# Kernel tuning notes

Measured on AMD Instinct MI355X. Metric: run time of the kernel, lower is better.

Reference implementation:

```python
import jax, jax.numpy as jnp
import numpy as np

B, T, F, U = 256, 2048, 64, 64
KEEP = 0.5  # recurrent_dropout=0.5 -> keep prob 0.5


def setup_inputs() -> dict:
    key = jax.random.key(0)
    ks = jax.random.split(key, 7)
    inputs = jax.random.normal(ks[0], (B, T, F), dtype=jnp.float32)
    kernel = jax.random.normal(ks[1], (F, 3 * U), dtype=jnp.float32) * 0.1
    recurrent_kernel = jax.random.normal(ks[2], (U, 3 * U), dtype=jnp.float32) * 0.1
    bias = jax.random.normal(ks[3], (2, 3 * U), dtype=jnp.float32) * 0.1
    dense_w = jax.random.normal(ks[4], (U, 1), dtype=jnp.float32) * 0.1
    dense_b = jnp.zeros((1,), dtype=jnp.float32)
    # Keras recurrent dropout: one fixed mask per gate (z, r, h), constant over time,
    # applied to h_prev before the recurrent matmul; inverted-dropout scaling.
    bern = jax.random.bernoulli(ks[5], KEEP, (3, B, U)).astype(jnp.float32)
    rec_mask = bern / KEEP
    return {
        "inputs": inputs,
        "kernel": kernel,
        "recurrent_kernel": recurrent_kernel,
        "bias": bias,
        "dense_w": dense_w,
        "dense_b": dense_b,
        "rec_mask": rec_mask,
    }


def _gru_dense(inputs, kernel, recurrent_kernel, bias, dense_w, dense_b, rec_mask):
    # Precompute input projections for all timesteps: [B, T, 3U]
    x_proj = jnp.einsum("btf,fg->btg", inputs, kernel) + bias[0]
    Uz, Ur, Uh = jnp.split(recurrent_kernel, 3, axis=1)  # each [U, U]
    bz, br, bh = jnp.split(bias[1], 3)                   # each [U]
    mz, mr, mh = rec_mask[0], rec_mask[1], rec_mask[2]   # each [B, U]

    def step(h, xt):
        xz, xr, xh = jnp.split(xt, 3, axis=-1)  # each [B, U]
        z = jax.nn.sigmoid(xz + (h * mz) @ Uz + bz)
        r = jax.nn.sigmoid(xr + (h * mr) @ Ur + br)
        hh = jnp.tanh(xh + r * ((h * mh) @ Uh + bh))  # reset_after=True
        h_new = z * h + (1.0 - z) * hh
        return h_new, None

    h0 = jnp.zeros((B, U), dtype=inputs.dtype)
    h_last, _ = jax.lax.scan(step, h0, jnp.swapaxes(x_proj, 0, 1))  # scan over T
    return h_last @ dense_w + dense_b  # [B, 1]


def reference(inputs, kernel, recurrent_kernel, bias, dense_w, dense_b, rec_mask):
    return _gru_dense(inputs, kernel, recurrent_kernel, bias, dense_w, dense_b, rec_mask)
```

## Files before the change

kernel.cpp:

```cpp
#include <hip/hip_runtime.h>

#define BB 256
#define TT 2048
#define FF 64
#define UU 64
#define C3 192
#define CH 32
#define NCH (TT / CH)

__device__ __forceinline__ float fast_sigmoid(float x) {
    return __builtin_amdgcn_rcpf(1.0f + __expf(-x));
}
__device__ __forceinline__ float fast_tanh(float x) {
    return 1.0f - 2.0f * __builtin_amdgcn_rcpf(__expf(2.0f * x) + 1.0f);
}
__device__ __forceinline__ float shflx(float v, int m) { return __shfl_xor(v, m, 64); }

#define REP16(M) M(0) M(1) M(2) M(3) M(4) M(5) M(6) M(7) \
                 M(8) M(9) M(10) M(11) M(12) M(13) M(14) M(15)

__global__ void __launch_bounds__(256, 1)
gru_v7(const float* __restrict__ in, const float* __restrict__ kmat,
       const float* __restrict__ rk, const float* __restrict__ bias,
       const float* __restrict__ mask, const float* __restrict__ dw,
       const float* __restrict__ db, float* __restrict__ out) {
    __shared__ __align__(16) float hb[2][64];
    __shared__ __align__(16) float ab[2][CH][FF];

    const int b    = blockIdx.x;
    const int lane = threadIdx.x & 63;
    const int wv   = threadIdx.x >> 6;
    const int sub  = lane >> 4;
    const int u    = lane & 15;
    const int j    = (wv << 4) + u;
    const int i0   = sub << 4;

    const float* mzp = mask;
    const float* mrp = mask + (size_t)BB * UU;
    const float* mhp = mask + (size_t)2 * BB * UU;
#define DECLW(K) float uz##K, ur##K, uh##K, kz##K, kr##K, kh##K;
    REP16(DECLW)
#define INITW(K) { const int i_ = i0 + (K); \
    uz##K = rk[i_ * C3 + j]       * mzp[(size_t)b * UU + i_]; \
    ur##K = rk[i_ * C3 + 64 + j]  * mrp[(size_t)b * UU + i_]; \
    uh##K = rk[i_ * C3 + 128 + j] * mhp[(size_t)b * UU + i_]; \
    kz##K = kmat[i_ * C3 + j]; \
    kr##K = kmat[i_ * C3 + 64 + j]; \
    kh##K = kmat[i_ * C3 + 128 + j]; }
    REP16(INITW)

    const float bzj  = bias[j]       + bias[C3 + j];
    const float brj  = bias[64 + j]  + bias[C3 + 64 + j];
    const float bh0j = bias[128 + j];
    const float bh1j = bias[C3 + 128 + j];

    const float* __restrict__ inb = in + (size_t)b * TT * FF;

    {
        const float* src = inb + (size_t)(wv * 8) * FF + lane;
        const float t0 = src[0 * FF], t1 = src[1 * FF], t2 = src[2 * FF],
                    t3 = src[3 * FF], t4 = src[4 * FF], t5 = src[5 * FF],
                    t6 = src[6 * FF], t7 = src[7 * FF];
        float* dst = &ab[0][wv * 8][lane];
        dst[0 * FF] = t0; dst[1 * FF] = t1; dst[2 * FF] = t2; dst[3 * FF] = t3;
        dst[4 * FF] = t4; dst[5 * FF] = t5; dst[6 * FF] = t6; dst[7 * FF] = t7;
    }
    if (wv == 0) hb[0][lane] = 0.0f;
    __syncthreads();

    float4 aA = *(const float4*)&ab[0][0][i0];
    float4 aB = *(const float4*)&ab[0][0][i0 + 4];
    float4 aC = *(const float4*)&ab[0][0][i0 + 8];
    float4 aD = *(const float4*)&ab[0][0][i0 + 12];

    float hown = 0.0f;

#pragma unroll 1
    for (int e = 0; e < TT; ++e) {
        const int  c  = e >> 5;
        const bool st = ((e & 31) == 0) && (c + 1 < NCH);

        float g0, g1, g2, g3, g4, g5, g6, g7;
        if (st) {
            const float* src = inb + ((size_t)(c + 1) * CH + wv * 8) * FF + lane;
            g0 = src[0 * FF]; g1 = src[1 * FF]; g2 = src[2 * FF]; g3 = src[3 * FF];
            g4 = src[4 * FF]; g5 = src[5 * FF]; g6 = src[6 * FF]; g7 = src[7 * FF];
        }

        const float4 hA = *(const float4*)&hb[e & 1][i0];
        const float4 hB = *(const float4*)&hb[e & 1][i0 + 4];
        const float4 hC = *(const float4*)&hb[e & 1][i0 + 8];
        const float4 hD = *(const float4*)&hb[e & 1][i0 + 12];

        float az = 0.f, ar = 0.f, axh = 0.f;
#define FMA_A(K, AV) { az = fmaf(AV, kz##K, az); ar = fmaf(AV, kr##K, ar); \
                       axh = fmaf(AV, kh##K, axh); }
        FMA_A(0,  aA.x) FMA_A(1,  aA.y) FMA_A(2,  aA.z) FMA_A(3,  aA.w)
        FMA_A(4,  aB.x) FMA_A(5,  aB.y) FMA_A(6,  aB.z) FMA_A(7,  aB.w)
        FMA_A(8,  aC.x) FMA_A(9,  aC.y) FMA_A(10, aC.z) FMA_A(11, aC.w)
        FMA_A(12, aD.x) FMA_A(13, aD.y) FMA_A(14, aD.z) FMA_A(15, aD.w)

        float hz = 0.f, hr = 0.f, hah = 0.f;
#define FMA_H(K, HV) { hz = fmaf(HV, uz##K, hz); hr = fmaf(HV, ur##K, hr); \
                       hah = fmaf(HV, uh##K, hah); }
        FMA_H(0,  hA.x) FMA_H(1,  hA.y) FMA_H(2,  hA.z) FMA_H(3,  hA.w)
        FMA_H(4,  hB.x) FMA_H(5,  hB.y) FMA_H(6,  hB.z) FMA_H(7,  hB.w)
        FMA_H(8,  hC.x) FMA_H(9,  hC.y) FMA_H(10, hC.z) FMA_H(11, hC.w)
        FMA_H(12, hD.x) FMA_H(13, hD.y) FMA_H(14, hD.z) FMA_H(15, hD.w)

        float sz = az + hz, sr = ar + hr, sxh = axh, sah = hah;
        { const float t0 = shflx(sz, 16), t1 = shflx(sr, 16),
                      t2 = shflx(sxh, 16), t3 = shflx(sah, 16);
          sz += t0; sr += t1; sxh += t2; sah += t3; }
        { const float t0 = shflx(sz, 32), t1 = shflx(sr, 32),
                      t2 = shflx(sxh, 32), t3 = shflx(sah, 32);
          sz += t0; sr += t1; sxh += t2; sah += t3; }

        const float z  = fast_sigmoid(sz + bzj);
        const float r  = fast_sigmoid(sr + brj);
        const float hh = fast_tanh(fmaf(r, sah + bh1j, sxh + bh0j));
        hown = fmaf(z, hown - hh, hh);

        if (sub == 0) hb[(e + 1) & 1][j] = hown;

        const int rn = (e + 1 < TT) ? (e + 1) : (TT - 1);
        const float* ap = &ab[(rn >> 5) & 1][rn & (CH - 1)][i0];
        aA = *(const float4*)(ap);
        aB = *(const float4*)(ap + 4);
        aC = *(const float4*)(ap + 8);
        aD = *(const float4*)(ap + 12);

        if (st) {
            float* dst = &ab[(c + 1) & 1][wv * 8][lane];
            dst[0 * FF] = g0; dst[1 * FF] = g1; dst[2 * FF] = g2; dst[3 * FF] = g3;
            dst[4 * FF] = g4; dst[5 * FF] = g5; dst[6 * FF] = g6; dst[7 * FF] = g7;
        }

        __syncthreads();
    }

    if (wv == 0) {
        float p = hb[0][lane] * dw[lane];
#pragma unroll
        for (int o = 32; o > 0; o >>= 1) p += __shfl_down(p, o, 64);
        if (lane == 0) out[b] = p + db[0];
    }
}

extern "C" void kernel_launch(void* const* d_in, const int* in_sizes, int n_in,
                              void* d_out, int out_size, void* d_ws, size_t ws_size,
                              hipStream_t stream) {
    (void)in_sizes; (void)n_in; (void)d_ws; (void)ws_size; (void)out_size;
    const float* inputs = (const float*)d_in[0];
    const float* kmat   = (const float*)d_in[1];
    const float* rk     = (const float*)d_in[2];
    const float* bias   = (const float*)d_in[3];
    const float* dw     = (const float*)d_in[4];
    const float* db     = (const float*)d_in[5];
    const float* mask   = (const float*)d_in[6];
    float* out = (float*)d_out;

    gru_v7<<<BB, 256, 0, stream>>>(inputs, kmat, rk, bias, mask, dw, db, out);
}
```

Baseline: 1.062 ms.

## Split input projection into a separate parallel kernel ahead of the recurrent scan

Computes the input projection x@K+bias for all timesteps in a separate wide-grid kernel that writes to workspace, in time chunks sized to fit the workspace. The scan kernel then only does the recurrent matmul per step and reads precomputed gate inputs from a shared-memory ring. This removes 48 FMAs per step from the serial critical path and frees registers. The cost is extra global traffic for the B*T*192 projection buffer and extra launches. If the workspace is too small it falls back to the fused kernel.

New measurement: 1.159 ms. +9.1%, slower.

```diff
diff --git a/kernel.cpp b/kernel.cpp
--- a/kernel.cpp
+++ b/kernel.cpp
@@ -5,9 +5,11 @@
 #define FF 64
 #define UU 64
 #define C3 192
-#define CH 32
-#define NCH (TT / CH)
-
+#define CH 16
+
+__device__ __forceinline__ float readlane_f(float v, int lane) {
+    return __int_as_float(__builtin_amdgcn_readlane(__float_as_int(v), lane));
+}
 __device__ __forceinline__ float fast_sigmoid(float x) {
     return __builtin_amdgcn_rcpf(1.0f + __expf(-x));
 }
@@ -18,14 +20,154 @@
 
 #define REP16(M) M(0) M(1) M(2) M(3) M(4) M(5) M(6) M(7) \
                  M(8) M(9) M(10) M(11) M(12) M(13) M(14) M(15)
+#define XREP8(M, I) M(I,0) M(I,1) M(I,2) M(I,3) M(I,4) M(I,5) M(I,6) M(I,7)
+#define XREP64(M) XREP8(M,0) XREP8(M,1) XREP8(M,2) XREP8(M,3) \
+                  XREP8(M,4) XREP8(M,5) XREP8(M,6) XREP8(M,7)
+
+__global__ __launch_bounds__(256)
+void xproj(const float* __restrict__ in, const float* __restrict__ kmat,
+           const float* __restrict__ bias, float* __restrict__ xp,
+           int t0, int tc) {
+    const int lane = threadIdx.x & 63;
+    const int wave = (int)((blockIdx.x * blockDim.x + threadIdx.x) >> 6);
+    const int nwaves = (int)((gridDim.x * blockDim.x) >> 6);
+
+#define DECLK(I,J) float kz_##I##J, kr_##I##J, kh_##I##J;
+    XREP64(DECLK)
+#define INITK(I,J) { const int f_ = (I)*8+(J); \
+    kz_##I##J = kmat[f_ * C3 + lane]; \
+    kr_##I##J = kmat[f_ * C3 + 64 + lane]; \
+    kh_##I##J = kmat[f_ * C3 + 128 + lane]; }
+    XREP64(INITK)
+
+    const float bz  = bias[lane]       + bias[C3 + lane];
+    const float br  = bias[64 + lane]  + bias[C3 + 64 + lane];
+    const float bh0 = bias[128 + lane];
+
+    const int rows = BB * tc;
+    for (int r = wave; r < rows; r += nwaves) {
+        const int bq = r / tc;
+        const int t  = t0 + (r - bq * tc);
+        const float a = in[((size_t)bq * TT + t) * FF + lane];
+        float az = bz, ar = br, ah = bh0;
+#define STEPK(I,J) { const float s_ = readlane_f(a, (I)*8+(J)); \
+        az = fmaf(s_, kz_##I##J, az); ar = fmaf(s_, kr_##I##J, ar); \
+        ah = fmaf(s_, kh_##I##J, ah); }
+        XREP64(STEPK)
+        float* o = xp + (size_t)r * C3;
+        o[lane] = az; o[64 + lane] = ar; o[128 + lane] = ah;
+    }
+}
 
 __global__ void __launch_bounds__(256, 1)
-gru_v7(const float* __restrict__ in, const float* __restrict__ kmat,
-       const float* __restrict__ rk, const float* __restrict__ bias,
-       const float* __restrict__ mask, const float* __restrict__ dw,
-       const float* __restrict__ db, float* __restrict__ out) {
+gru_scan(const float* __restrict__ xp, const float* __restrict__ rk,
+         const float* __restrict__ bias, const float* __restrict__ mask,
+         const float* __restrict__ dw, const float* __restrict__ db,
+         float* __restrict__ hws, float* __restrict__ out,
+         int tc, int first, int last) {
     __shared__ __align__(16) float hb[2][64];
-    __shared__ __align__(16) float ab[2][CH][FF];
+    __shared__ __align__(16) float ring[2][CH][C3];
+
+    const int b    = blockIdx.x;
+    const int tid  = threadIdx.x;
+    const int lane = tid & 63;
+    const int wv   = tid >> 6;
+    const int sub  = lane >> 4;
+    const int u    = lane & 15;
+    const int j    = (wv << 4) + u;
+    const int i0   = sub << 4;
+
+    const float* mzp = mask;
+    const float* mrp = mask + (size_t)BB * UU;
+    const float* mhp = mask + (size_t)2 * BB * UU;
+#define DECLUW(K) float uz##K, ur##K, uh##K;
+    REP16(DECLUW)
+#define INITUW(K) { const int i_ = i0 + (K); \
+    uz##K = rk[i_ * C3 + j]       * mzp[(size_t)b * UU + i_]; \
+    ur##K = rk[i_ * C3 + 64 + j]  * mrp[(size_t)b * UU + i_]; \
+    uh##K = rk[i_ * C3 + 128 + j] * mhp[(size_t)b * UU + i_]; }
+    REP16(INITUW)
+
+    const float bh1j = bias[C3 + 128 + j];
+
+    const float* __restrict__ xpb = xp + (size_t)b * tc * C3;
+
+    {
+        const float4* src = (const float4*)xpb;
+        const float4 v0 = src[tid], v1 = src[tid + 256], v2 = src[tid + 512];
+        float4* dst = (float4*)&ring[0][0][0];
+        dst[tid] = v0; dst[tid + 256] = v1; dst[tid + 512] = v2;
+    }
+    float hown = first ? 0.0f : hws[(size_t)b * UU + j];
+    if (wv == 0) hb[0][lane] = first ? 0.0f : hws[(size_t)b * UU + lane];
+    __syncthreads();
+
+#pragma unroll 1
+    for (int e = 0; e < tc; ++e) {
+        const int  c  = e >> 4;
+        const bool st = ((e & 15) == 0) && ((c + 1) * CH < tc);
+
+        float4 g0, g1, g2;
+        if (st) {
+            const float4* src = (const float4*)(xpb + (size_t)(c + 1) * CH * C3);
+            g0 = src[tid]; g1 = src[tid + 256]; g2 = src[tid + 512];
+        }
+
+        const float4 hA = *(const float4*)&hb[e & 1][i0];
+        const float4 hB = *(const float4*)&hb[e & 1][i0 + 4];
+        const float4 hC = *(const float4*)&hb[e & 1][i0 + 8];
+        const float4 hD = *(const float4*)&hb[e & 1][i0 + 12];
+
+        const float* xrow = &ring[c & 1][e & 15][0];
+        const float xz = xrow[j], xr = xrow[64 + j], xh = xrow[128 + j];
+
+        float hz = 0.f, hr = 0.f, hah = 0.f;
+#define FMA_H(K, HV) { hz = fmaf(HV, uz##K, hz); hr = fmaf(HV, ur##K, hr); \
+                       hah = fmaf(HV, uh##K, hah); }
+        FMA_H(0,  hA.x) FMA_H(1,  hA.y) FMA_H(2,  hA.z) FMA_H(3,  hA.w)
+        FMA_H(4,  hB.x) FMA_H(5,  hB.y) FMA_H(6,  hB.z) FMA_H(7,  hB.w)
+        FMA_H(8,  hC.x) FMA_H(9,  hC.y) FMA_H(10, hC.z) FMA_H(11, hC.w)
+        FMA_H(12, hD.x) FMA_H(13, hD.y) FMA_H(14, hD.z) FMA_H(15, hD.w)
+
+        float sz = hz, sr = hr, sah = hah;
+        { const float t0 = shflx(sz, 16), t1 = shflx(sr, 16), t2 = shflx(sah, 16);
+          sz += t0; sr += t1; sah += t2; }
+        { const float t0 = shflx(sz, 32), t1 = shflx(sr, 32), t2 = shflx(sah, 32);
+          sz += t0; sr += t1; sah += t2; }
+
+        const float z  = fast_sigmoid(sz + xz);
+        const float r  = fast_sigmoid(sr + xr);
+        const float hh = fast_tanh(fmaf(r, sah + bh1j, xh));
+        hown = fmaf(z, hown - hh, hh);
+
+        if (sub == 0) hb[(e + 1) & 1][j] = hown;
+
+        if (st) {
+            float4* dst = (float4*)&ring[(c + 1) & 1][0][0];
+            dst[tid] = g0; dst[tid + 256] = g1; dst[tid + 512] = g2;
+        }
+        __syncthreads();
+    }
+
+    if (last) {
+        if (wv == 0) {
+            float p = hb[tc & 1][lane] * dw[lane];
+#pragma unroll
+            for (int o = 32; o > 0; o >>= 1) p += __shfl_down(p, o, 64);
+            if (lane == 0) out[b] = p + db[0];
+        }
+    } else {
+        if (wv == 0) hws[(size_t)b * UU + lane] = hb[tc & 1][lane];
+    }
+}
+
+__global__ void __launch_bounds__(256, 1)
+gru_fused7(const float* __restrict__ in, const float* __restrict__ kmat,
+           const float* __restrict__ rk, const float* __restrict__ bias,
+           const float* __restrict__ mask, const float* __restrict__ dw,
+           const float* __restrict__ db, float* __restrict__ out) {
+    __shared__ __align__(16) float hb[2][64];
+    __shared__ __align__(16) float ab[2][32][FF];
 
     const int b    = blockIdx.x;
     const int lane = threadIdx.x & 63;
@@ -38,16 +180,16 @@
     const float* mzp = mask;
     const float* mrp = mask + (size_t)BB * UU;
     const float* mhp = mask + (size_t)2 * BB * UU;
-#define DECLW(K) float uz##K, ur##K, uh##K, kz##K, kr##K, kh##K;
-    REP16(DECLW)
-#define INITW(K) { const int i_ = i0 + (K); \
-    uz##K = rk[i_ * C3 + j]       * mzp[(size_t)b * UU + i_]; \
-    ur##K = rk[i_ * C3 + 64 + j]  * mrp[(size_t)b * UU + i_]; \
-    uh##K = rk[i_ * C3 + 128 + j] * mhp[(size_t)b * UU + i_]; \
-    kz##K = kmat[i_ * C3 + j]; \
-    kr##K = kmat[i_ * C3 + 64 + j]; \
-    kh##K = kmat[i_ * C3 + 128 + j]; }
-    REP16(INITW)
+#define DECLW7(K) float fuz##K, fur##K, fuh##K, fkz##K, fkr##K, fkh##K;
+    REP16(DECLW7)
+#define INITW7(K) { const int i_ = i0 + (K); \
+    fuz##K = rk[i_ * C3 + j]       * mzp[(size_t)b * UU + i_]; \
+    fur##K = rk[i_ * C3 + 64 + j]  * mrp[(size_t)b * UU + i_]; \
+    fuh##K = rk[i_ * C3 + 128 + j] * mhp[(size_t)b * UU + i_]; \
+    fkz##K = kmat[i_ * C3 + j]; \
+    fkr##K = kmat[i_ * C3 + 64 + j]; \
+    fkh##K = kmat[i_ * C3 + 128 + j]; }
+    REP16(INITW7)
 
     const float bzj  = bias[j]       + bias[C3 + j];
     const float brj  = bias[64 + j]  + bias[C3 + 64 + j];
@@ -55,7 +197,6 @@
     const float bh1j = bias[C3 + 128 + j];
 
     const float* __restrict__ inb = in + (size_t)b * TT * FF;
-
     {
         const float* src = inb + (size_t)(wv * 8) * FF + lane;
         const float t0 = src[0 * FF], t1 = src[1 * FF], t2 = src[2 * FF],
@@ -72,41 +213,38 @@
     float4 aB = *(const float4*)&ab[0][0][i0 + 4];
     float4 aC = *(const float4*)&ab[0][0][i0 + 8];
     float4 aD = *(const float4*)&ab[0][0][i0 + 12];
-
     float hown = 0.0f;
 
 #pragma unroll 1
     for (int e = 0; e < TT; ++e) {
         const int  c  = e >> 5;
-        const bool st = ((e & 31) == 0) && (c + 1 < NCH);
-
+        const bool st = ((e & 31) == 0) && (c + 1 < TT / 32);
         float g0, g1, g2, g3, g4, g5, g6, g7;
         if (st) {
-            const float* src = inb + ((size_t)(c + 1) * CH + wv * 8) * FF + lane;
+            const float* src = inb + ((size_t)(c + 1) * 32 + wv * 8) * FF + lane;
             g0 = src[0 * FF]; g1 = src[1 * FF]; g2 = src[2 * FF]; g3 = src[3 * FF];
             g4 = src[4 * FF]; g5 = src[5 * FF]; g6 = src[6 * FF]; g7 = src[7 * FF];
         }
-
         const float4 hA = *(const float4*)&hb[e & 1][i0];
         const float4 hB = *(const float4*)&hb[e & 1][i0 + 4];
         const float4 hC = *(const float4*)&hb[e & 1][i0 + 8];
         const float4 hD = *(const float4*)&hb[e & 1][i0 + 12];
 
         float az = 0.f, ar = 0.f, axh = 0.f;
-#define FMA_A(K, AV) { az = fmaf(AV, kz##K, az); ar = fmaf(AV, kr##K, ar); \
-                       axh = fmaf(AV, kh##K, axh); }
-        FMA_A(0,  aA.x) FMA_A(1,  aA.y) FMA_A(2,  aA.z) FMA_A(3,  aA.w)
-        FMA_A(4,  aB.x) FMA_A(5,  aB.y) FMA_A(6,  aB.z) FMA_A(7,  aB.w)
-        FMA_A(8,  aC.x) FMA_A(9,  aC.y) FMA_A(10, aC.z) FMA_A(11, aC.w)
-        FMA_A(12, aD.x) FMA_A(13, aD.y) FMA_A(14, aD.z) FMA_A(15, aD.w)
+#define FMA_A7(K, AV) { az = fmaf(AV, fkz##K, az); ar = fmaf(AV, fkr##K, ar); \
+                        axh = fmaf(AV, fkh##K, axh); }
+        FMA_A7(0,  aA.x) FMA_A7(1,  aA.y) FMA_A7(2,  aA.z) FMA_A7(3,  aA.w)
+        FMA_A7(4,  aB.x) FMA_A7(5,  aB.y) FMA_A7(6,  aB.z) FMA_A7(7,  aB.w)
+        FMA_A7(8,  aC.x) FMA_A7(9,  aC.y) FMA_A7(10, aC.z) FMA_A7(11, aC.w)
+        FMA_A7(12, aD.x) FMA_A7(13, aD.y) FMA_A7(14, aD.z) FMA_A7(15, aD.w)
 
         float hz = 0.f, hr = 0.f, hah = 0.f;
-#define FMA_H(K, HV) { hz = fmaf(HV, uz##K, hz); hr = fmaf(HV, ur##K, hr); \
-                       hah = fmaf(HV, uh##K, hah); }
-        FMA_H(0,  hA.x) FMA_H(1,  hA.y) FMA_H(2,  hA.z) FMA_H(3,  hA.w)
-        FMA_H(4,  hB.x) FMA_H(5,  hB.y) FMA_H(6,  hB.z) FMA_H(7,  hB.w)
-        FMA_H(8,  hC.x) FMA_H(9,  hC.y) FMA_H(10, hC.z) FMA_H(11, hC.w)
-        FMA_H(12, hD.x) FMA_H(13, hD.y) FMA_H(14, hD.z) FMA_H(15, hD.w)
+#define FMA_H7(K, HV) { hz = fmaf(HV, fuz##K, hz); hr = fmaf(HV, fur##K, hr); \
+                        hah = fmaf(HV, fuh##K, hah); }
+        FMA_H7(0,  hA.x) FMA_H7(1,  hA.y) FMA_H7(2,  hA.z) FMA_H7(3,  hA.w)
+        FMA_H7(4,  hB.x) FMA_H7(5,  hB.y) FMA_H7(6,  hB.z) FMA_H7(7,  hB.w)
+        FMA_H7(8,  hC.x) FMA_H7(9,  hC.y) FMA_H7(10, hC.z) FMA_H7(11, hC.w)
+        FMA_H7(12, hD.x) FMA_H7(13, hD.y) FMA_H7(14, hD.z) FMA_H7(15, hD.w)
 
         float sz = az + hz, sr = ar + hr, sxh = axh, sah = hah;
         { const float t0 = shflx(sz, 16), t1 = shflx(sr, 16),
@@ -120,11 +258,10 @@
         const float r  = fast_sigmoid(sr + brj);
         const float hh = fast_tanh(fmaf(r, sah + bh1j, sxh + bh0j));
         hown = fmaf(z, hown - hh, hh);
-
         if (sub == 0) hb[(e + 1) & 1][j] = hown;
 
         const int rn = (e + 1 < TT) ? (e + 1) : (TT - 1);
-        const float* ap = &ab[(rn >> 5) & 1][rn & (CH - 1)][i0];
+        const float* ap = &ab[(rn >> 5) & 1][rn & 31][i0];
         aA = *(const float4*)(ap);
         aB = *(const float4*)(ap + 4);
         aC = *(const float4*)(ap + 8);
@@ -135,7 +272,6 @@
             dst[0 * FF] = g0; dst[1 * FF] = g1; dst[2 * FF] = g2; dst[3 * FF] = g3;
             dst[4 * FF] = g4; dst[5 * FF] = g5; dst[6 * FF] = g6; dst[7 * FF] = g7;
         }
-
         __syncthreads();
     }
 
@@ -150,7 +286,7 @@
 extern "C" void kernel_launch(void* const* d_in, const int* in_sizes, int n_in,
                               void* d_out, int out_size, void* d_ws, size_t ws_size,
                               hipStream_t stream) {
-    (void)in_sizes; (void)n_in; (void)d_ws; (void)ws_size; (void)out_size;
+    (void)in_sizes; (void)n_in; (void)out_size;
     const float* inputs = (const float*)d_in[0];
     const float* kmat   = (const float*)d_in[1];
     const float* rk     = (const float*)d_in[2];
@@ -160,5 +296,30 @@
     const float* mask   = (const float*)d_in[6];
     float* out = (float*)d_out;
 
-    gru_v7<<<BB, 256, 0, stream>>>(inputs, kmat, rk, bias, mask, dw, db, out);
-}
+    const size_t h_bytes   = (size_t)BB * UU * sizeof(float);
+    const size_t row_bytes = (size_t)BB * C3 * sizeof(float);
+
+    int cap = 0;
+    if (ws_size > h_bytes)
+        cap = (int)((ws_size - h_bytes) / row_bytes) & ~(CH - 1);
+    if (cap > TT) cap = TT;
+
+    if (cap >= 256) {
+        float* hws = (float*)d_ws;
+        float* xp  = (float*)((char*)d_ws + h_bytes);
+        const int nch  = (TT + cap - 1) / cap;
+        int base = (TT + nch - 1) / nch;
+        base = (base + CH - 1) & ~(CH - 1);
+        int t0 = 0;
+        while (t0 < TT) {
+            const int cur = (TT - t0) < base ? (TT - t0) : base;
+            xproj<<<512, 256, 0, stream>>>(inputs, kmat, bias, xp, t0, cur);
+            gru_scan<<<BB, 256, 0, stream>>>(xp, rk, bias, mask, dw, db, hws, out,
+                                             cur, t0 == 0 ? 1 : 0,
+                                             (t0 + cur == TT) ? 1 : 0);
+            t0 += cur;
+        }
+    } else {
+        gru_fused7<<<BB, 256, 0, stream>>>(inputs, kmat, rk, bias, mask, dw, db, out);
+    }
+}
```
